# Kernel optimization log

Measured on AMD Instinct MI355X. Metric: run time of the kernel, lower is better.

## Reference

```python
import jax, jax.numpy as jnp
import numpy as np

B, S, E = 4, 2048, 768
DFF = 4 * E
EPS = 1e-5


def _layernorm(x, g, b):
    mu = jnp.mean(x, axis=-1, keepdims=True)
    var = jnp.mean(jnp.square(x - mu), axis=-1, keepdims=True)
    return (x - mu) * jax.lax.rsqrt(var + EPS) * g + b


def setup_inputs() -> dict:
    key = jax.random.key(0)
    ks = jax.random.split(key, 16)
    w = lambda k, shp: jax.random.normal(k, shp, dtype=jnp.float32) * 0.02
    inp = {
        "x": jax.random.normal(ks[0], (B, S, E), dtype=jnp.float32),
        "kv": jax.random.normal(ks[1], (B, S, E), dtype=jnp.float32),
        "wq_w": w(ks[2], (E, E)), "wq_b": jnp.zeros((E,), jnp.float32),
        "wk_w": w(ks[3], (E, E)), "wk_b": jnp.zeros((E,), jnp.float32),
        "wv_w": w(ks[4], (E, E)), "wv_b": jnp.zeros((E,), jnp.float32),
        "ln1_g": jnp.ones((E,), jnp.float32), "ln1_b": jnp.zeros((E,), jnp.float32),
        "wq2_w": w(ks[5], (E, E)), "wq2_b": jnp.zeros((E,), jnp.float32),
        "wk2_w": w(ks[6], (E, E)), "wk2_b": jnp.zeros((E,), jnp.float32),
        "wv2_w": w(ks[7], (E, E)), "wv2_b": jnp.zeros((E,), jnp.float32),
        "ln2_g": jnp.ones((E,), jnp.float32), "ln2_b": jnp.zeros((E,), jnp.float32),
        "w1": w(ks[8], (DFF, E)), "b1": jnp.zeros((DFF,), jnp.float32),
        "w2": w(ks[9], (E, DFF)), "b2": jnp.zeros((E,), jnp.float32),
        "ln3_g": jnp.ones((E,), jnp.float32), "ln3_b": jnp.zeros((E,), jnp.float32),
    }
    return inp


def reference(x, kv, wq_w, wq_b, wk_w, wk_b, wv_w, wv_b, ln1_g, ln1_b,
              wq2_w, wq2_b, wk2_w, wk2_b, wv2_w, wv2_b, ln2_g, ln2_b,
              w1, b1, w2, b2, ln3_g, ln3_b):
    scalar = 1.0 / np.sqrt(E).astype(np.float32)
    mask_value = jnp.finfo(x.dtype).min
    s = x.shape[1]
    causal = jnp.triu(jnp.ones((s, s), dtype=bool), k=1)  # True above diagonal -> masked

    # ---- causal self-attention (single head, full E) ----
    q = x @ wq_w.T + wq_b
    k = x @ wk_w.T + wk_b
    v = x @ wv_w.T + wv_b
    scores = jnp.einsum('bqe,bke->bqk', q, k) * scalar
    scores = jnp.where(causal, mask_value, scores)
    h1 = jnp.einsum('bqk,bke->bqe', jax.nn.softmax(scores, axis=-1), v)
    x = _layernorm(x + h1, ln1_g, ln1_b)

    # ---- cross-attention over kv (no mask) ----
    q2 = x @ wq2_w.T + wq2_b
    k2 = kv @ wk2_w.T + wk2_b
    v2 = kv @ wv2_w.T + wv2_b
    scores2 = jnp.einsum('bqe,bke->bqk', q2, k2) * scalar
    h2 = jnp.einsum('bqk,bke->bqe', jax.nn.softmax(scores2, axis=-1), v2)
    x = _layernorm(x + h2, ln2_g, ln2_b)

    # ---- MLP: Linear -> ReLU -> Linear -> ReLU (note trailing ReLU) ----
    h = jax.nn.relu(x @ w1.T + b1)
    mlp = jax.nn.relu(h @ w2.T + b2)
    return _layernorm(x + mlp, ln3_g, ln3_b)
```

## Files before the change

### kernel.cpp

```cpp
#include <hip/hip_runtime.h>
#include <hip/hip_bf16.h>
#include <math.h>


typedef __bf16 bf16_t;
typedef bf16_t bf16x4 __attribute__((ext_vector_type(4)));
typedef bf16_t bf16x8 __attribute__((ext_vector_type(8)));
typedef float f32x4 __attribute__((ext_vector_type(4)));

struct MMDesc {
    const bf16_t* A;
    const bf16_t* B;
    const float* bias;
    __hip_bfloat16* C;
    float* lsum;
    int koff;
    int trans;
};
struct MMArgs { MMDesc g[8]; };

__device__ __forceinline__ int xcd_swz(int bid, int nwg) {
    const int q = nwg >> 3, r = nwg & 7;
    const int xcd = bid & 7, o = bid >> 3;
    const int base = (xcd < r) ? xcd * (q + 1) : r * (q + 1) + (xcd - r) * q;
    return base + o;
}

__device__ __forceinline__ void load16(const bf16_t* g, bf16_t* l) {
    __builtin_amdgcn_global_load_lds(
        (const __attribute__((address_space(1))) unsigned int*)g,
        (__attribute__((address_space(3))) unsigned int*)l, 16, 0, 0);
}

__device__ __forceinline__ void rd4h(const bf16_t* p0, const bf16_t* p1, int H,
                                     bf16x8 f[4][2]) {
#pragma unroll
    for (int i = 0; i < 4; ++i) {
        f[i][0] = *(const bf16x8*)(p0 + H + i * 1024);
        f[i][1] = *(const bf16x8*)(p1 + H + i * 1024);
    }
}
__device__ __forceinline__ void rd2h(const bf16_t* p0, const bf16_t* p1, int H,
                                     bf16x8 f[2][2]) {
#pragma unroll
    for (int i = 0; i < 2; ++i) {
        f[i][0] = *(const bf16x8*)(p0 + H + i * 1024);
        f[i][1] = *(const bf16x8*)(p1 + H + i * 1024);
    }
}

#define SBAR asm volatile("s_barrier" ::: "memory")
#define SCH  __builtin_amdgcn_sched_barrier(0)
#define PBAR do { SCH; SBAR; SCH; } while (0)
#define PRIO1 __builtin_amdgcn_s_setprio(1)
#define PRIO0 __builtin_amdgcn_s_setprio(0)
#define VMC6 asm volatile("s_waitcnt vmcnt(6)" ::: "memory")
#define LGK8 do { asm volatile("s_waitcnt lgkmcnt(8)" ::: "memory"); } while (0)

#define QMFMA(mh, nh, BF) do { \
    _Pragma("unroll") \
    for (int ks = 0; ks < 2; ++ks) \
    _Pragma("unroll") \
    for (int mi = 0; mi < 4; ++mi) \
    _Pragma("unroll") \
    for (int ni = 0; ni < 2; ++ni) \
        acc[(mh) * 4 + mi][(nh) * 2 + ni] = __builtin_amdgcn_mfma_f32_16x16x32_bf16( \
            af[mi][ks], BF[ni][ks], acc[(mh) * 4 + mi][(nh) * 2 + ni], 0, 0, 0); \
} while (0)

__device__ __forceinline__ void mm8_core(
    const bf16_t* Ag, const bf16_t* Bg, int lda, int ldb, int K,
    bf16_t* lds, int w, int l, f32x4 acc[8][4])
{
    const long ldal = lda, ldbl = ldb;
    const int fr = l & 15, kq = l >> 4;
    const int rr = w * 8 + (l >> 3);
    const int c8e = ((l & 7) ^ (l >> 3)) * 8;
    const bf16_t* pA[2];
    const bf16_t* pB[2];
    pA[0] = Ag + (long)rr * ldal + c8e;
    pA[1] = pA[0] + 128 * ldal;
    pB[0] = Bg + (long)rr * ldbl + c8e;
    pB[1] = pB[0] + 128 * ldbl;
    const int s0 = ((0 + kq) ^ (fr & 7)) * 8;
    const int s1 = ((4 + kq) ^ (fr & 7)) * 8;
    const int arow = ((w >> 2) * 64 + fr) * 64;
    const int brow = ((w & 3) * 32 + fr) * 64;
    const bf16_t* lA0s0 = lds + arow + s0;
    const bf16_t* lA0s1 = lds + arow + s1;
    const bf16_t* lA1s0 = lds + 32768 + arow + s0;
    const bf16_t* lA1s1 = lds + 32768 + arow + s1;
    const bf16_t* lB0s0 = lds + 16384 + brow + s0;
    const bf16_t* lB0s1 = lds + 16384 + brow + s1;
    const bf16_t* lB1s0 = lds + 49152 + brow + s0;
    const bf16_t* lB1s1 = lds + 49152 + brow + s1;
    bf16_t* stA = lds + w * 512;
    bf16_t* stB = lds + 16384 + w * 512;

    auto stg = [&](int b, int isB, int h, int t) {
        const bf16_t* g = (isB ? pB[h] : pA[h]) + (long)t * 64;
        bf16_t* d = (isB ? stB : stA) + b * 32768 + h * 8192;
        load16(g, d);
        load16(g + 64 * (isB ? ldbl : ldal), d + 4096);
    };

    bf16x8 af[4][2], bf0[2][2], bf1[2][2];
    const int NT = K >> 6, NI = NT >> 1;

    stg(0, 0, 0, 0); stg(0, 1, 0, 0); stg(0, 1, 1, 0); stg(0, 0, 1, 0);
    stg(1, 0, 0, 1); stg(1, 1, 0, 1); stg(1, 1, 1, 1);
    VMC6;
    SBAR; SCH;

    for (int i = 0; i < NI; ++i) {
        const int t1 = 2 * i + 1;
        int t2 = 2 * i + 2; if (t2 >= NT) t2 -= 2;
        int t3 = 2 * i + 3; if (t3 >= NT) t3 -= 2;
        rd4h(lA0s0, lA0s1, 0, af); rd2h(lB0s0, lB0s1, 0, bf0);
        stg(1, 0, 1, t1);
        LGK8;
        PBAR; PRIO1; QMFMA(0, 0, bf0); PRIO0;
        rd2h(lB0s0, lB0s1, 8192, bf1);
        PBAR; PRIO1; QMFMA(0, 1, bf1); PRIO0;
        rd4h(lA0s0, lA0s1, 8192, af);
        stg(0, 0, 0, t2); stg(0, 1, 0, t2);
        PBAR; PRIO1; QMFMA(1, 0, bf0); PRIO0;
        stg(0, 1, 1, t2);
        VMC6;
        PBAR; PRIO1; QMFMA(1, 1, bf1); PRIO0;
        rd4h(lA1s0, lA1s1, 0, af); rd2h(lB1s0, lB1s1, 0, bf0);
        stg(0, 0, 1, t2);
        LGK8;
        PBAR; PRIO1; QMFMA(0, 0, bf0); PRIO0;
        rd2h(lB1s0, lB1s1, 8192, bf1);
        PBAR; PRIO1; QMFMA(0, 1, bf1); PRIO0;
        rd4h(lA1s0, lA1s1, 8192, af);
        stg(1, 0, 0, t3); stg(1, 1, 0, t3);
        PBAR; PRIO1; QMFMA(1, 0, bf0); PRIO0;
        stg(1, 1, 1, t3);
        VMC6;
        PBAR; PRIO1; QMFMA(1, 1, bf1); PRIO0;
    }
    asm volatile("s_waitcnt vmcnt(0)" ::: "memory");
    SBAR; SCH;
}

template <bool RELU, bool CLAMPK>
__global__ __launch_bounds__(512, 2) void mm8_std(
    MMArgs args, int M, int N, int K, int lda, int ldb, float scale, int GX)
{
    __shared__ __align__(16) bf16_t lds[65536];
    const MMDesc dsc = args.g[blockIdx.z];

    const int lin = xcd_swz(blockIdx.x, gridDim.x);
    const int panel = lin / (8 * GX);
    const int rem = lin - panel * 8 * GX;
    const int bx = rem >> 3;
    const int by = panel * 8 + (rem & 7);
    const int m0 = by * 256, n0 = bx * 256;
    const int tid = threadIdx.x, w = tid >> 6, l = tid & 63;

    f32x4 acc[8][4];
    const f32x4 z4 = {0.f, 0.f, 0.f, 0.f};
#pragma unroll
    for (int i = 0; i < 8; ++i)
#pragma unroll
        for (int j = 0; j < 4; ++j) acc[i][j] = z4;

    int Keff = K;
    if (CLAMPK) {
        int km = (by + 1) * 256 - dsc.koff;
        Keff = km < K ? km : K;
    }
    if (!CLAMPK || Keff > 0)
        mm8_core(dsc.A + (long)m0 * lda, dsc.B + (long)n0 * ldb,
                 lda, ldb, Keff, lds, w, l, acc);

    const int fr = l & 15, erow = (l >> 4) * 4;
    const int wrow = (w >> 2) * 64, wcol = (w & 3) * 32;
    bf16_t* ctb = lds;
    __hip_bfloat16* ct = (__hip_bfloat16*)lds;
#pragma unroll
    for (int mh = 0; mh < 2; ++mh) {
        if (mh) __syncthreads();
#pragma unroll
        for (int nh = 0; nh < 2; ++nh)
#pragma unroll
            for (int ni = 0; ni < 2; ++ni) {
                const int cl = nh * 128 + wcol + ni * 16 + fr;
                const float bv = dsc.bias ? dsc.bias[n0 + cl] : 0.f;
#pragma unroll
                for (int mi = 0; mi < 4; ++mi) {
                    const int lr = wrow + mi * 16 + erow;
                    const f32x4 a = acc[mh * 4 + mi][nh * 2 + ni];
                    if (dsc.trans) {
                        bf16x4 p;
#pragma unroll
                        for (int r = 0; r < 4; ++r) {
                            float v = a[r] * scale + bv;
                            if (RELU) v = fmaxf(v, 0.f);
                            p[r] = (bf16_t)v;
                        }
                        *(bf16x4*)(ctb + cl * 140 + lr) = p;
                    } else {
#pragma unroll
                        for (int r = 0; r < 4; ++r) {
                            float v = a[r] * scale + bv;
                            if (RELU) v = fmaxf(v, 0.f);
                            ct[(lr + r) * 264 + cl] = __float2bfloat16(v);
                        }
                    }
                }
            }
        __syncthreads();
        if (dsc.trans) {
            __hip_bfloat16* base = dsc.C + ((long)(m0 >> 11) * N + n0) * 2048
                                 + (m0 & 2047) + mh * 128;
#pragma unroll
            for (int u = 0; u < 8; ++u) {
                const int e = u * 4096 + tid * 8;
                const int rl = e >> 7, cl = e & 127;
                const bf16_t* src = ctb + rl * 140 + cl;
                const uint2 lo = *(const uint2*)(src);
                const uint2 hi = *(const uint2*)(src + 4);
                const uint4 v = {lo.x, lo.y, hi.x, hi.y};
                *(uint4*)(base + (long)rl * 2048 + cl) = v;
            }
        } else {
            __hip_bfloat16* base = dsc.C + (long)(m0 + mh * 128) * N + n0;
#pragma unroll
            for (int u = 0; u < 8; ++u) {
                const int e = u * 4096 + tid * 8;
                *(uint4*)(base + (long)(e >> 8) * N + (e & 255))
                    = *(const uint4*)(ct + (e >> 8) * 264 + (e & 255));
            }
        }
    }
}

template <bool CAUSAL>
__global__ __launch_bounds__(512, 2) void mm8_exp(
    MMArgs args, int N, int K, int lda, int ldb, float scale, int GX)
{
    __shared__ __align__(16) bf16_t lds[65536];
    const MMDesc dsc = args.g[blockIdx.z];

    int bx, by;
    if (CAUSAL) {
        const int t = xcd_swz(blockIdx.x, gridDim.x);
        by = (int)((sqrtf(8.f * t + 1.f) - 1.f) * 0.5f);
        while ((by + 1) * (by + 2) / 2 <= t) ++by;
        while (by * (by + 1) / 2 > t) --by;
        bx = t - by * (by + 1) / 2;
    } else {
        const int lin = xcd_swz(blockIdx.x, gridDim.x);
        const int panel = lin / (8 * GX);
        const int rem = lin - panel * 8 * GX;
        bx = rem >> 3;
        by = panel * 8 + (rem & 7);
    }
    const int m0 = by * 256, n0 = bx * 256;
    const int tid = threadIdx.x, w = tid >> 6, l = tid & 63;

    f32x4 acc[8][4];
    const f32x4 z4 = {0.f, 0.f, 0.f, 0.f};
#pragma unroll
    for (int i = 0; i < 8; ++i)
#pragma unroll
        for (int j = 0; j < 4; ++j) acc[i][j] = z4;

    mm8_core(dsc.A + (long)m0 * lda, dsc.B + (long)n0 * ldb,
             lda, ldb, K, lds, w, l, acc);

    const int fr = l & 15, erow = (l >> 4) * 4;
    const int wrow = (w >> 2) * 64, wcol = (w & 3) * 32;
    __hip_bfloat16* ct = (__hip_bfloat16*)lds;
#pragma unroll
    for (int mh = 0; mh < 2; ++mh) {
        if (mh) __syncthreads();
#pragma unroll
        for (int mi = 0; mi < 4; ++mi) {
            const int lr = wrow + mi * 16 + erow;
#pragma unroll
            for (int r = 0; r < 4; ++r) {
                const int grow = m0 + mh * 128 + lr + r;
                float rs = 0.f;
#pragma unroll
                for (int nh = 0; nh < 2; ++nh)
#pragma unroll
                    for (int ni = 0; ni < 2; ++ni) {
                        const int cl = nh * 128 + wcol + ni * 16 + fr;
                        float e;
                        if (CAUSAL && (n0 + cl) > grow)
                            e = 0.f;
                        else
                            e = __expf(acc[mh * 4 + mi][nh * 2 + ni][r] * scale);
                        ct[(lr + r) * 264 + cl] = __float2bfloat16(e);
                        rs += e;
                    }
#pragma unroll
                for (int o = 8; o > 0; o >>= 1) rs += __shfl_down(rs, o, 16);
                if ((l & 15) == 0) atomicAdd(&dsc.lsum[grow], rs);
            }
        }
        __syncthreads();
        __hip_bfloat16* base = dsc.C + (long)(m0 + mh * 128) * N + n0;
#pragma unroll
        for (int u = 0; u < 8; ++u) {
            const int e = u * 4096 + tid * 8;
            *(uint4*)(base + (long)(e >> 8) * N + (e & 255))
                = *(const uint4*)(ct + (e >> 8) * 264 + (e & 255));
        }
    }
}

__device__ __forceinline__ float waveReduceSum(float v) {
#pragma unroll
    for (int o = 32; o > 0; o >>= 1) v += __shfl_down(v, o, 64);
    return v;
}
__device__ __forceinline__ float blockReduceSum(float v, float* s) {
    int lane = threadIdx.x & 63, w = threadIdx.x >> 6;
    v = waveReduceSum(v);
    __syncthreads();
    if (lane == 0) s[w] = v;
    __syncthreads();
    return s[0] + s[1] + s[2] + s[3];
}

template <bool BR, bool XF32>
__global__ __launch_bounds__(256) void ln_kernel(
    const float* __restrict__ xf, const __hip_bfloat16* __restrict__ xh,
    const __hip_bfloat16* __restrict__ h1, const __hip_bfloat16* __restrict__ h2,
    const float* __restrict__ hbias, const float* __restrict__ lsum,
    const float* __restrict__ g, const float* __restrict__ beta,
    float* __restrict__ outf, __hip_bfloat16* __restrict__ outb) {
    __shared__ float red[4];
    const int E = 768;
    const long row = blockIdx.x;
    const float hscale = lsum ? (1.f / lsum[row]) : 1.f;

    float vals[3];
    float sum = 0.f;
#pragma unroll
    for (int i = 0; i < 3; ++i) {
        int c = threadIdx.x + i * 256;
        float t = __bfloat162float(h1[row * E + c]) + __bfloat162float(h2[row * E + c]);
        if (BR) t = fmaxf(t + hbias[c], 0.f);
        else t *= hscale;
        float xv = XF32 ? xf[row * E + c] : __bfloat162float(xh[row * E + c]);
        vals[i] = xv + t;
        sum += vals[i];
    }
    sum = blockReduceSum(sum, red);
    const float mean = sum * (1.f / 768.f);

    float ss = 0.f;
#pragma unroll
    for (int i = 0; i < 3; ++i) {
        float d = vals[i] - mean;
        ss += d * d;
    }
    ss = blockReduceSum(ss, red);
    const float inv = rsqrtf(ss * (1.f / 768.f) + 1e-5f);

#pragma unroll
    for (int i = 0; i < 3; ++i) {
        int c = threadIdx.x + i * 256;
        float v = (vals[i] - mean) * inv * g[c] + beta[c];
        if (outf) outf[row * E + c] = v;
        if (outb) outb[row * E + c] = __float2bfloat16(v);
    }
}

struct CvtPtrs {
    const float* s[10];
    __hip_bfloat16* d[10];
    float* zero;
};
__global__ __launch_bounds__(256) void cvt_all(CvtPtrs p) {
    int bid = blockIdx.x, seg, off;
    if (bid >= 20352) {
        int i = (bid - 20352) * 1024 + threadIdx.x * 4;
        float4 z = {0.f, 0.f, 0.f, 0.f};
        *(float4*)(p.zero + i) = z;
        return;
    }
    if (bid < 3456) {
        seg = bid / 576;
        off = (bid % 576) * 1024;
    } else if (bid < 8064) {
        int t = bid - 3456;
        seg = 6 + t / 2304;
        off = (t % 2304) * 1024;
    } else {
        int t = bid - 8064;
        seg = 8 + t / 6144;
        off = (t % 6144) * 1024;
    }
    const float* s = p.s[seg];
    __hip_bfloat16* d = p.d[seg];
    int i = off + threadIdx.x * 4;
    float4 v = *(const float4*)(s + i);
    d[i + 0] = __float2bfloat16(v.x);
    d[i + 1] = __float2bfloat16(v.y);
    d[i + 2] = __float2bfloat16(v.z);
    d[i + 3] = __float2bfloat16(v.w);
}

extern "C" void kernel_launch(void* const* d_in, const int* in_sizes, int n_in,
                              void* d_out, int out_size, void* d_ws, size_t ws_size,
                              hipStream_t stream) {
    const int Bb = 4, S = 2048, E = 768, DFF = 3072;
    const int Nr = Bb * S;

    const float* x    = (const float*)d_in[0];
    const float* kv   = (const float*)d_in[1];
    const float* wq_w = (const float*)d_in[2];
    const float* wq_b = (const float*)d_in[3];
    const float* wk_w = (const float*)d_in[4];
    const float* wk_b = (const float*)d_in[5];
    const float* wv_w = (const float*)d_in[6];
    const float* wv_b = (const float*)d_in[7];
    const float* ln1g = (const float*)d_in[8];
    const float* ln1b = (const float*)d_in[9];
    const float* wq2w = (const float*)d_in[10];
    const float* wq2b = (const float*)d_in[11];
    const float* wk2w = (const float*)d_in[12];
    const float* wk2b = (const float*)d_in[13];
    const float* wv2w = (const float*)d_in[14];
    const float* wv2b = (const float*)d_in[15];
    const float* ln2g = (const float*)d_in[16];
    const float* ln2b = (const float*)d_in[17];
    const float* w1   = (const float*)d_in[18];
    const float* b1   = (const float*)d_in[19];
    const float* w2   = (const float*)d_in[20];
    const float* b2   = (const float*)d_in[21];
    const float* ln3g = (const float*)d_in[22];
    const float* ln3b = (const float*)d_in[23];
    float* out = (float*)d_out;

    char* wsp = (char*)d_ws;
    auto alloc = [&](size_t bytes) {
        char* p = wsp;
        wsp += (bytes + 255) & ~(size_t)255;
        return p;
    };
    const size_t nSE = (size_t)Nr * E;
    const size_t nSS = (size_t)Bb * S * S;
    __hip_bfloat16* Pb   = (__hip_bfloat16*)alloc(nSS * 2);
    __hip_bfloat16* qb   = (__hip_bfloat16*)alloc(nSE * 2);
    __hip_bfloat16* kb   = (__hip_bfloat16*)alloc(nSE * 2);
    __hip_bfloat16* hffb = Pb;
    __hip_bfloat16* vtb  = (__hip_bfloat16*)alloc(nSE * 2);
    __hip_bfloat16* xb   = (__hip_bfloat16*)alloc(nSE * 2);
    __hip_bfloat16* kvb  = (__hip_bfloat16*)alloc(nSE * 2);
    __hip_bfloat16* actb = (__hip_bfloat16*)alloc(nSE * 2);
    __hip_bfloat16* hA   = (__hip_bfloat16*)alloc(nSE * 2);
    __hip_bfloat16* hB   = (__hip_bfloat16*)alloc(nSE * 2);
    __hip_bfloat16* wqb   = (__hip_bfloat16*)alloc((size_t)E * E * 2);
    __hip_bfloat16* wkb   = (__hip_bfloat16*)alloc((size_t)E * E * 2);
    __hip_bfloat16* wvb   = (__hip_bfloat16*)alloc((size_t)E * E * 2);
    __hip_bfloat16* wq2bm = (__hip_bfloat16*)alloc((size_t)E * E * 2);
    __hip_bfloat16* wk2bm = (__hip_bfloat16*)alloc((size_t)E * E * 2);
    __hip_bfloat16* wv2bm = (__hip_bfloat16*)alloc((size_t)E * E * 2);
    __hip_bfloat16* w1b   = (__hip_bfloat16*)alloc((size_t)DFF * E * 2);
    __hip_bfloat16* w2b   = (__hip_bfloat16*)alloc((size_t)E * DFF * 2);
    float* lsum1 = (float*)alloc((size_t)Nr * 4);
    float* lsum2 = (float*)alloc((size_t)Nr * 4);

    __hip_bfloat16* k2b  = (__hip_bfloat16*)d_out;
    __hip_bfloat16* vtb2 = k2b + nSE;

    const float scale = 1.0f / sqrtf((float)E);
    const dim3 blk(256);
    const dim3 blk5(512);

    CvtPtrs cp;
    cp.s[0] = wq_w; cp.d[0] = wqb;
    cp.s[1] = wk_w; cp.d[1] = wkb;
    cp.s[2] = wv_w; cp.d[2] = wvb;
    cp.s[3] = wq2w; cp.d[3] = wq2bm;
    cp.s[4] = wk2w; cp.d[4] = wk2bm;
    cp.s[5] = wv2w; cp.d[5] = wv2bm;
    cp.s[6] = w1;   cp.d[6] = w1b;
    cp.s[7] = w2;   cp.d[7] = w2b;
    cp.s[8] = x;    cp.d[8] = xb;
    cp.s[9] = kv;   cp.d[9] = kvb;
    cp.zero = lsum1;
    cvt_all<<<8064 + 12288 + 16, blk, 0, stream>>>(cp);

    {
        MMArgs a{};
        a.g[0] = {(const bf16_t*)xb,  (const bf16_t*)wqb,   wq_b, qb,   nullptr, 0, 0};
        a.g[1] = {(const bf16_t*)xb,  (const bf16_t*)wkb,   wk_b, kb,   nullptr, 0, 0};
        a.g[2] = {(const bf16_t*)xb,  (const bf16_t*)wvb,   wv_b, vtb,  nullptr, 0, 1};
        a.g[3] = {(const bf16_t*)kvb, (const bf16_t*)wk2bm, wk2b, k2b,  nullptr, 0, 0};
        a.g[4] = {(const bf16_t*)kvb, (const bf16_t*)wv2bm, wv2b, vtb2, nullptr, 0, 1};
        mm8_std<false, false><<<dim3(96, 1, 5), blk5, 0, stream>>>(
            a, Nr, E, E, E, E, 1.f, 3);
    }
    {
        MMArgs a{};
        for (int b = 0; b < 4; ++b)
            a.g[b] = {(const bf16_t*)qb + (long)b * S * E,
                      (const bf16_t*)kb + (long)b * S * E, nullptr,
                      Pb + (long)b * S * S, lsum1 + b * S, 0, 0};
        mm8_exp<true><<<dim3(36, 1, 4), blk5, 0, stream>>>(a, S, E, E, E, scale, 8);
    }
    {
        MMArgs a{};
        for (int b = 0; b < 4; ++b)
            for (int ks = 0; ks < 2; ++ks)
                a.g[b * 2 + ks] = {(const bf16_t*)Pb + (long)b * S * S + ks * 1024,
                                   (const bf16_t*)vtb + (long)b * E * S + ks * 1024,
                                   nullptr, (ks ? hB : hA) + (long)b * S * E,
                                   nullptr, ks * 1024, 0};
        mm8_std<false, true><<<dim3(24, 1, 8), blk5, 0, stream>>>(
            a, S, E, 1024, S, S, 1.f, 3);
    }
    ln_kernel<false, false><<<Nr, blk, 0, stream>>>(
        nullptr, xb, hA, hB, nullptr, lsum1, ln1g, ln1b, nullptr, actb);

    {
        MMArgs a{};
        a.g[0] = {(const bf16_t*)actb, (const bf16_t*)wq2bm, wq2b, qb, nullptr, 0, 0};
        mm8_std<false, false><<<dim3(96, 1, 1), blk5, 0, stream>>>(
            a, Nr, E, E, E, E, 1.f, 3);
    }
    {
        MMArgs a{};
        for (int b = 0; b < 4; ++b)
            a.g[b] = {(const bf16_t*)qb + (long)b * S * E,
                      (const bf16_t*)k2b + (long)b * S * E, nullptr,
                      Pb + (long)b * S * S, lsum2 + b * S, 0, 0};
        mm8_exp<false><<<dim3(64, 1, 4), blk5, 0, stream>>>(a, S, E, E, E, scale, 8);
    }
    {
        MMArgs a{};
        for (int b = 0; b < 4; ++b)
            for (int ks = 0; ks < 2; ++ks)
                a.g[b * 2 + ks] = {(const bf16_t*)Pb + (long)b * S * S + ks * 1024,
                                   (const bf16_t*)vtb2 + (long)b * E * S + ks * 1024,
                                   nullptr, (ks ? hB : hA) + (long)b * S * E,
                                   nullptr, 0, 0};
        mm8_std<false, false><<<dim3(24, 1, 8), blk5, 0, stream>>>(
            a, S, E, 1024, S, S, 1.f, 3);
    }
    ln_kernel<false, false><<<Nr, blk, 0, stream>>>(
        nullptr, actb, hA, hB, nullptr, lsum2, ln2g, ln2b, nullptr, actb);

    {
        MMArgs a{};
        a.g[0] = {(const bf16_t*)actb, (const bf16_t*)w1b, b1, hffb, nullptr, 0, 0};
        mm8_std<true, false><<<dim3(384, 1, 1), blk5, 0, stream>>>(
            a, Nr, DFF, E, E, E, 1.f, 12);
    }
    {
        MMArgs a{};
        a.g[0] = {(const bf16_t*)hffb, (const bf16_t*)w2b, nullptr, hA, nullptr, 0, 0};
        a.g[1] = {(const bf16_t*)hffb + 1536, (const bf16_t*)w2b + 1536, nullptr,
                  hB, nullptr, 0, 0};
        mm8_std<false, false><<<dim3(96, 1, 2), blk5, 0, stream>>>(
            a, Nr, E, 1536, DFF, DFF, 1.f, 3);
    }
    ln_kernel<true, false><<<Nr, blk, 0, stream>>>(
        nullptr, actb, hA, hB, b2, nullptr, ln3g, ln3b, out, nullptr);
}
```

Baseline: 502.0 us.

## Restructure GEMM main loop with ping-pong LDS fragment registers and fewer barriers

Rewrites the inner K-loop of the shared 256x256 GEMM core. It now reads A and B fragments per k-slice into double register buffers (a0/a1, b0/b1) and issues 16 MFMAs per phase, using sched_group_barrier to interleave LDS reads with MFMAs. This replaces the eight barrier-separated quarter blocks per iteration with two barriers, aiming to cut synchronisation and expose more overlap of LDS reads with matrix math. The cost is higher register pressure, and the vmcnt(0) waits before each barrier may stall on outstanding global-to-LDS loads.

```diff
diff --git a/kernel.cpp b/kernel.cpp
--- a/kernel.cpp
+++ b/kernel.cpp
@@ -32,40 +32,35 @@
         (__attribute__((address_space(3))) unsigned int*)l, 16, 0, 0);
 }
 
-__device__ __forceinline__ void rd4h(const bf16_t* p0, const bf16_t* p1, int H,
-                                     bf16x8 f[4][2]) {
-#pragma unroll
-    for (int i = 0; i < 4; ++i) {
-        f[i][0] = *(const bf16x8*)(p0 + H + i * 1024);
-        f[i][1] = *(const bf16x8*)(p1 + H + i * 1024);
-    }
-}
-__device__ __forceinline__ void rd2h(const bf16_t* p0, const bf16_t* p1, int H,
-                                     bf16x8 f[2][2]) {
-#pragma unroll
-    for (int i = 0; i < 2; ++i) {
-        f[i][0] = *(const bf16x8*)(p0 + H + i * 1024);
-        f[i][1] = *(const bf16x8*)(p1 + H + i * 1024);
-    }
-}
-
 #define SBAR asm volatile("s_barrier" ::: "memory")
 #define SCH  __builtin_amdgcn_sched_barrier(0)
-#define PBAR do { SCH; SBAR; SCH; } while (0)
 #define PRIO1 __builtin_amdgcn_s_setprio(1)
 #define PRIO0 __builtin_amdgcn_s_setprio(0)
-#define VMC6 asm volatile("s_waitcnt vmcnt(6)" ::: "memory")
-#define LGK8 do { asm volatile("s_waitcnt lgkmcnt(8)" ::: "memory"); } while (0)
-
-#define QMFMA(mh, nh, BF) do { \
+#define VMC0 asm volatile("s_waitcnt vmcnt(0)" ::: "memory")
+
+#define RDA(dst, base, H) do { \
     _Pragma("unroll") \
-    for (int ks = 0; ks < 2; ++ks) \
+    for (int i_ = 0; i_ < 4; ++i_) \
+        dst[i_] = *(const bf16x8*)((base) + (H) + i_ * 1024); \
+} while (0)
+#define RDB(dst, base) do { \
+    dst[0] = *(const bf16x8*)(base); \
+    dst[1] = *(const bf16x8*)((base) + 1024); \
+    dst[2] = *(const bf16x8*)((base) + 8192); \
+    dst[3] = *(const bf16x8*)((base) + 8192 + 1024); \
+} while (0)
+#define CL16(mh, A_, B_) do { \
     _Pragma("unroll") \
     for (int mi = 0; mi < 4; ++mi) \
     _Pragma("unroll") \
-    for (int ni = 0; ni < 2; ++ni) \
-        acc[(mh) * 4 + mi][(nh) * 2 + ni] = __builtin_amdgcn_mfma_f32_16x16x32_bf16( \
-            af[mi][ks], BF[ni][ks], acc[(mh) * 4 + mi][(nh) * 2 + ni], 0, 0, 0); \
+    for (int nj = 0; nj < 4; ++nj) \
+        acc[(mh) * 4 + mi][nj] = __builtin_amdgcn_mfma_f32_16x16x32_bf16( \
+            A_[mi], B_[nj], acc[(mh) * 4 + mi][nj], 0, 0, 0); \
+} while (0)
+#define PH(nr) do { \
+    __builtin_amdgcn_sched_group_barrier(0x100, nr, 0); \
+    __builtin_amdgcn_sched_group_barrier(0x008, 16, 0); \
+    SCH; \
 } while (0)
 
 __device__ __forceinline__ void mm8_core(
@@ -86,14 +81,14 @@
     const int s1 = ((4 + kq) ^ (fr & 7)) * 8;
     const int arow = ((w >> 2) * 64 + fr) * 64;
     const int brow = ((w & 3) * 32 + fr) * 64;
-    const bf16_t* lA0s0 = lds + arow + s0;
-    const bf16_t* lA0s1 = lds + arow + s1;
-    const bf16_t* lA1s0 = lds + 32768 + arow + s0;
-    const bf16_t* lA1s1 = lds + 32768 + arow + s1;
-    const bf16_t* lB0s0 = lds + 16384 + brow + s0;
-    const bf16_t* lB0s1 = lds + 16384 + brow + s1;
-    const bf16_t* lB1s0 = lds + 49152 + brow + s0;
-    const bf16_t* lB1s1 = lds + 49152 + brow + s1;
+    const bf16_t* A00 = lds + arow + s0;
+    const bf16_t* A01 = lds + arow + s1;
+    const bf16_t* A10 = lds + 32768 + arow + s0;
+    const bf16_t* A11 = lds + 32768 + arow + s1;
+    const bf16_t* B00 = lds + 16384 + brow + s0;
+    const bf16_t* B01 = lds + 16384 + brow + s1;
+    const bf16_t* B10 = lds + 49152 + brow + s0;
+    const bf16_t* B11 = lds + 49152 + brow + s1;
     bf16_t* stA = lds + w * 512;
     bf16_t* stB = lds + 16384 + w * 512;
 
@@ -104,44 +99,54 @@
         load16(g + 64 * (isB ? ldbl : ldal), d + 4096);
     };
 
-    bf16x8 af[4][2], bf0[2][2], bf1[2][2];
+    bf16x8 a0[4], a1[4], b0[4], b1[4];
     const int NT = K >> 6, NI = NT >> 1;
 
-    stg(0, 0, 0, 0); stg(0, 1, 0, 0); stg(0, 1, 1, 0); stg(0, 0, 1, 0);
-    stg(1, 0, 0, 1); stg(1, 1, 0, 1); stg(1, 1, 1, 1);
-    VMC6;
+    stg(0, 0, 0, 0); stg(0, 1, 0, 0); stg(0, 0, 1, 0); stg(0, 1, 1, 0);
+    stg(1, 0, 0, 1); stg(1, 1, 0, 1);
+    asm volatile("s_waitcnt vmcnt(4)" ::: "memory");
     SBAR; SCH;
+    RDA(a0, A00, 0); RDB(b0, B00);
+    SCH;
 
     for (int i = 0; i < NI; ++i) {
-        const int t1 = 2 * i + 1;
-        int t2 = 2 * i + 2; if (t2 >= NT) t2 -= 2;
-        int t3 = 2 * i + 3; if (t3 >= NT) t3 -= 2;
-        rd4h(lA0s0, lA0s1, 0, af); rd2h(lB0s0, lB0s1, 0, bf0);
-        stg(1, 0, 1, t1);
-        LGK8;
-        PBAR; PRIO1; QMFMA(0, 0, bf0); PRIO0;
-        rd2h(lB0s0, lB0s1, 8192, bf1);
-        PBAR; PRIO1; QMFMA(0, 1, bf1); PRIO0;
-        rd4h(lA0s0, lA0s1, 8192, af);
-        stg(0, 0, 0, t2); stg(0, 1, 0, t2);
-        PBAR; PRIO1; QMFMA(1, 0, bf0); PRIO0;
-        stg(0, 1, 1, t2);
-        VMC6;
-        PBAR; PRIO1; QMFMA(1, 1, bf1); PRIO0;
-        rd4h(lA1s0, lA1s1, 0, af); rd2h(lB1s0, lB1s1, 0, bf0);
-        stg(0, 0, 1, t2);
-        LGK8;
-        PBAR; PRIO1; QMFMA(0, 0, bf0); PRIO0;
-        rd2h(lB1s0, lB1s1, 8192, bf1);
-        PBAR; PRIO1; QMFMA(0, 1, bf1); PRIO0;
-        rd4h(lA1s0, lA1s1, 8192, af);
-        stg(1, 0, 0, t3); stg(1, 1, 0, t3);
-        PBAR; PRIO1; QMFMA(1, 0, bf0); PRIO0;
-        stg(1, 1, 1, t3);
-        VMC6;
-        PBAR; PRIO1; QMFMA(1, 1, bf1); PRIO0;
-    }
-    asm volatile("s_waitcnt vmcnt(0)" ::: "memory");
+        const int tn1 = 2 * i + 1;
+        int tn2 = 2 * i + 2; if (tn2 >= NT) tn2 -= 2;
+        int tn3 = 2 * i + 3; if (tn3 >= NT) tn3 -= 2;
+        RDA(a1, A01, 0); RDB(b1, B01);
+        stg(1, 0, 1, tn1); stg(1, 1, 1, tn1);
+        PRIO1; CL16(0, a0, b0); PRIO0;
+        PH(8);
+        RDA(a0, A00, 8192);
+        PRIO1; CL16(0, a1, b1); PRIO0;
+        PH(4);
+        RDA(a1, A01, 8192);
+        PRIO1; CL16(1, a0, b0); PRIO0;
+        PH(4);
+        VMC0;
+        SBAR; SCH;
+        stg(0, 0, 0, tn2); stg(0, 1, 0, tn2);
+        RDA(a0, A10, 0); RDB(b0, B10);
+        PRIO1; CL16(1, a1, b1); PRIO0;
+        PH(8);
+        RDA(a1, A11, 0); RDB(b1, B11);
+        stg(0, 0, 1, tn2); stg(0, 1, 1, tn2);
+        PRIO1; CL16(0, a0, b0); PRIO0;
+        PH(8);
+        RDA(a0, A10, 8192);
+        PRIO1; CL16(0, a1, b1); PRIO0;
+        PH(4);
+        RDA(a1, A11, 8192);
+        PRIO1; CL16(1, a0, b0); PRIO0;
+        PH(4);
+        VMC0;
+        SBAR; SCH;
+        stg(1, 0, 0, tn3); stg(1, 1, 0, tn3);
+        RDA(a0, A00, 0); RDB(b0, B00);
+        PRIO1; CL16(1, a1, b1); PRIO0;
+        PH(8);
+    }
+    VMC0;
     SBAR; SCH;
 }
 
```

New measurement: 495.9 us. No clear change (-1.2%).
